# Optimization experiments

Hardware: AMD Instinct MI355X
Metric: run time of the kernel (lower is better)

## Reference

```python
import jax, jax.numpy as jnp
import numpy as np

NUM_CLASSES = 512  # P distinct identities in the batch (labels are in [0, P))
TAU = 0.5
EPS = 1e-12


def _l2norm(x):
    # F.normalize(x, dim=1) with eps clamp
    n = jnp.sqrt(jnp.sum(x * x, axis=1, keepdims=True))
    return x / jnp.maximum(n, EPS)


def setup_inputs() -> dict:
    key = jax.random.key(0)
    k1, k2, k3 = jax.random.split(key, 3)
    N, D, P = 8192, 2048, NUM_CLASSES
    feat_vp = jax.random.normal(k1, (N, D), dtype=jnp.float32)
    feat_ap = jax.random.normal(k2, (N, D), dtype=jnp.float32)
    feat_rp = jax.random.normal(k3, (N, D), dtype=jnp.float32)
    # P identities, K = N/P instances each; every class present
    label = (jnp.arange(N) % P).astype(jnp.int32)
    return {"feat_vp": feat_vp, "feat_ap": feat_ap, "feat_rp": feat_rp, "label": label}


def reference(feat_vp, feat_ap, feat_rp, label):
    P = NUM_CLASSES
    fv = _l2norm(feat_vp)
    fa = _l2norm(feat_ap)
    fr = _l2norm(feat_rp)

    # segment-mean over labels (replaces the O(N^2 D) python loop)
    counts = jax.ops.segment_sum(jnp.ones_like(label, dtype=fv.dtype), label,
                                 num_segments=P)  # [P]
    inv_cnt = 1.0 / counts[:, None]

    def centers(f):
        s = jax.ops.segment_sum(f, label, num_segments=P)  # [P, D]
        return _l2norm(s * inv_cnt)

    cv, ca, cr = centers(fv), centers(fa), centers(fr)

    # per-sample centers = unique centers gathered back by label
    loss_intra = (jnp.sum((fv - cv[label]) ** 2, axis=1).mean()
                  + jnp.sum((fa - ca[label]) ** 2, axis=1).mean()
                  + jnp.sum((fr - cr[label]) ** 2, axis=1).mean())

    def pair_loss(c1, c2):
        logits = (c1 @ c2.T) / TAU  # [P, P]
        logp = jax.nn.log_softmax(logits, axis=1)
        return -jnp.mean(jnp.diagonal(logp))

    loss_inter = pair_loss(cv, ca) + pair_loss(cv, cr) + pair_loss(ca, cr)
    return loss_intra + loss_inter
```

## Files before the change

kernel.cpp:

```cpp
#include <hip/hip_runtime.h>
#include <hip/hip_bf16.h>

#define P_CLS 512
#define D_DIM 2048
#define CAP   32
#define TAU_INV 2.0f

typedef short short8 __attribute__((ext_vector_type(8)));
typedef float f32x4 __attribute__((ext_vector_type(4)));

__device__ __forceinline__ unsigned short f2bf_bits(float x) {
  __hip_bfloat16 b = __float2bfloat16(x);
  unsigned short u;
  __builtin_memcpy(&u, &b, sizeof(u));
  return u;
}

__device__ __forceinline__ void async16(const void* g, void* l) {
  __builtin_amdgcn_global_load_lds(
      (const __attribute__((address_space(1))) void*)g,
      (__attribute__((address_space(3))) void*)l, 16, 0, 0);
}

__device__ __forceinline__ float xred_sum(float v) {
#pragma unroll
  for (int o = 1; o < 64; o <<= 1) v += __shfl_xor(v, o, 64);
  return v;
}
__device__ __forceinline__ float xred_max(float v) {
#pragma unroll
  for (int o = 1; o < 64; o <<= 1) v = fmaxf(v, __shfl_xor(v, o, 64));
  return v;
}

__global__ void k_init(int* cnt, float* accs) {
  int t = blockIdx.x * blockDim.x + threadIdx.x;
  if (t < P_CLS) cnt[t] = 0;
  if (t < 8) accs[t] = 0.f;
}

__global__ void k_index(const int* __restrict__ label, int* __restrict__ cnt,
                        int* __restrict__ idx, int n) {
  int i = blockIdx.x * blockDim.x + threadIdx.x;
  if (i < n) {
    int p = label[i];
    int slot = atomicAdd(&cnt[p], 1);
    if (slot < CAP) idx[p * CAP + slot] = i;
  }
}

__global__ __launch_bounds__(256)
void k_centers(const float* __restrict__ f0, const float* __restrict__ f1,
               const float* __restrict__ f2, const int* __restrict__ cnt,
               const int* __restrict__ idx, __hip_bfloat16* __restrict__ cb,
               float* __restrict__ accs) {
  __shared__ __align__(16) float rows[8 * D_DIM];
  __shared__ float scr[16];
  int p = blockIdx.x, m = blockIdx.y;
  const float* F = (m == 0) ? f0 : (m == 1) ? f1 : f2;
  int t = threadIdx.x, lane = t & 63, wv = t >> 6;
  int c = cnt[p];
  if (c > CAP) c = CAP;
  const int* idxp = idx + p * CAP;

  f32x4 acc0 = {0, 0, 0, 0}, acc1 = {0, 0, 0, 0};
  for (int base = 0; base < c; base += 8) {
#pragma unroll
    for (int s = 0; s < 2; ++s) {
      int rr = 2 * wv + s, gr = base + rr;
      if (gr < c) {
        const char* rowp = (const char*)(F + (long)idxp[gr] * D_DIM);
        char* ldsp = (char*)(rows + rr * D_DIM);
#pragma unroll
        for (int j = 0; j < 8; ++j)
          async16(rowp + j * 1024 + lane * 16, ldsp + j * 1024 + lane * 16);
      }
    }
    __syncthreads();
#pragma unroll
    for (int s = 0; s < 2; ++s) {
      int rr = 2 * wv + s;
      const f32x4* rp = (const f32x4*)(rows + rr * D_DIM);
      float ssq = 0.f;
#pragma unroll
      for (int j = 0; j < 8; ++j) {
        f32x4 q = rp[lane + 64 * j];
        q = q * q;
        ssq += q.x + q.y + q.z + q.w;
      }
      ssq = xred_sum(ssq);
      if (lane == 0)
        scr[rr] = (base + rr < c) ? (1.0f / fmaxf(sqrtf(ssq), 1e-12f)) : 0.f;
    }
    __syncthreads();
#pragma unroll
    for (int rr = 0; rr < 8; ++rr) {
      float w = scr[rr];
      f32x4 x0 = *(const f32x4*)(rows + rr * D_DIM + t * 4);
      f32x4 x1 = *(const f32x4*)(rows + rr * D_DIM + 1024 + t * 4);
      acc0 += x0 * w;
      acc1 += x1 * w;
    }
    __syncthreads();
  }
  f32x4 q0 = acc0 * acc0, q1 = acc1 * acc1;
  float s2 = q0.x + q0.y + q0.z + q0.w + q1.x + q1.y + q1.z + q1.w;
  s2 = xred_sum(s2);
  if (lane == 0) scr[8 + wv] = s2;
  __syncthreads();
  s2 = scr[8] + scr[9] + scr[10] + scr[11];
  float sn = sqrtf(s2);
  float inv = 1.0f / fmaxf(sn, 1e-12f);
  __hip_bfloat16* dst = cb + ((long)m * P_CLS + p) * D_DIM;
  f32x4 o0 = acc0 * inv, o1 = acc1 * inv;
  ushort4 h0, h1;
  h0.x = f2bf_bits(o0.x); h0.y = f2bf_bits(o0.y);
  h0.z = f2bf_bits(o0.z); h0.w = f2bf_bits(o0.w);
  h1.x = f2bf_bits(o1.x); h1.y = f2bf_bits(o1.y);
  h1.z = f2bf_bits(o1.z); h1.w = f2bf_bits(o1.w);
  ((ushort4*)dst)[t] = h0;
  ((ushort4*)dst)[t + 256] = h1;
  if (t == 0 && c > 0) atomicAdd(&accs[0], sn);
}

__global__ __launch_bounds__(256)
void k_gemm(const __hip_bfloat16* __restrict__ cbh, float* __restrict__ logits) {
  __shared__ __align__(16) unsigned short As[2][64 * 40], Bs[2][64 * 40];
  int pair = blockIdx.y, kz = blockIdx.z, nkz = gridDim.z;
  int ksl = D_DIM / nkz;
  int ma = (pair == 2) ? 1 : 0;
  int mb = (pair == 0) ? 1 : 2;
  const unsigned short* A =
      (const unsigned short*)cbh + (long)ma * P_CLS * D_DIM + kz * ksl;
  const unsigned short* B =
      (const unsigned short*)cbh + (long)mb * P_CLS * D_DIM + kz * ksl;
  float* C = logits + ((long)kz * 3 + pair) * P_CLS * P_CLS;
  int tm = (blockIdx.x >> 3) * 64, tn = (blockIdx.x & 7) * 64;
  int t = threadIdx.x, lane = t & 63, wv = t >> 6;
  int srow = t >> 2, skc = (t & 3) * 8;
  int quad = lane >> 4, mr = lane & 15;
  const unsigned short* pa = A + (long)(tm + srow) * D_DIM + skc;
  const unsigned short* pb = B + (long)(tn + srow) * D_DIM + skc;
  f32x4 acc[4] = {{0,0,0,0},{0,0,0,0},{0,0,0,0},{0,0,0,0}};
  uint4 av = *(const uint4*)pa, bv = *(const uint4*)pb;
  *(uint4*)(&As[0][srow * 40 + skc]) = av;
  *(uint4*)(&Bs[0][srow * 40 + skc]) = bv;
  av = *(const uint4*)(pa + 32); bv = *(const uint4*)(pb + 32);
  const int NIT = ksl / 32;
  for (int it = 0; it < NIT; ++it) {
    __syncthreads();
    int cur = it & 1;
    if (it + 1 < NIT) {
      *(uint4*)(&As[cur ^ 1][srow * 40 + skc]) = av;
      *(uint4*)(&Bs[cur ^ 1][srow * 40 + skc]) = bv;
    }
    if (it + 2 < NIT) {
      av = *(const uint4*)(pa + (it + 2) * 32);
      bv = *(const uint4*)(pb + (it + 2) * 32);
    }
    short8 af = *(const short8*)(&As[cur][(wv * 16 + mr) * 40 + quad * 8]);
#pragma unroll
    for (int nb = 0; nb < 4; ++nb) {
      short8 bfr = *(const short8*)(&Bs[cur][(nb * 16 + mr) * 40 + quad * 8]);
      acc[nb] = __builtin_amdgcn_mfma_f32_16x16x32_bf16(af, bfr, acc[nb], 0, 0, 0);
    }
  }
  int crow = tm + wv * 16 + quad * 4;
#pragma unroll
  for (int nb = 0; nb < 4; ++nb)
#pragma unroll
    for (int r = 0; r < 4; ++r)
      C[(long)(crow + r) * P_CLS + tn + nb * 16 + mr] = acc[nb][r] * TAU_INV;
}

__global__ __launch_bounds__(256)
void k_lse(const float* __restrict__ logits, float* __restrict__ accs, int nkz) {
  __shared__ float sred[8];
  int row = blockIdx.x;
  int p = row & (P_CLS - 1);
  int t = threadIdx.x, lane = t & 63, wv = t >> 6;
  float v0 = 0.f, v1 = 0.f, diag = 0.f;
  for (int z = 0; z < nkz; ++z) {
    const float* L = logits + ((long)z * 3 * P_CLS + row) * P_CLS;
    v0 += L[t];
    v1 += L[t + 256];
  }
  float mx = xred_max(fmaxf(v0, v1));
  if (lane == 0) sred[wv] = mx;
  __syncthreads();
  mx = fmaxf(fmaxf(sred[0], sred[1]), fmaxf(sred[2], sred[3]));
  float e = expf(v0 - mx) + expf(v1 - mx);
  e = xred_sum(e);
  if (lane == 0) sred[4 + wv] = e;
  __syncthreads();
  if (t == 0) {
    float tot = sred[4] + sred[5] + sred[6] + sred[7];
    for (int z = 0; z < nkz; ++z)
      diag += logits[((long)z * 3 * P_CLS + row) * P_CLS + p];
    atomicAdd(&accs[1], mx + logf(tot) - diag);
  }
}

__global__ void k_final(const float* __restrict__ accs, float* __restrict__ out,
                        float invN) {
  out[0] = 6.0f - 2.0f * invN * accs[0] + accs[1] * (1.0f / (float)P_CLS);
}

extern "C" void kernel_launch(void* const* d_in, const int* in_sizes, int n_in,
                              void* d_out, int out_size, void* d_ws, size_t ws_size,
                              hipStream_t stream) {
  const float* fvp = (const float*)d_in[0];
  const float* fap = (const float*)d_in[1];
  const float* frp = (const float*)d_in[2];
  const int* label = (const int*)d_in[3];
  int N = in_sizes[3];

  char* ws = (char*)d_ws;
  int* cnt = (int*)ws;
  int* idx = (int*)(ws + 2048);
  float* accs = (float*)(ws + 2048 + 65536);
  __hip_bfloat16* cb = (__hip_bfloat16*)(ws + 131072);
  float* logits = (float*)(ws + 131072 + 3ul * P_CLS * D_DIM * 2);

  size_t base = 131072 + 3ul * P_CLS * D_DIM * 2;
  size_t per_z = 3ul * P_CLS * P_CLS * 4;
  int KZ = (ws_size >= base + 4 * per_z) ? 4 : 2;

  hipLaunchKernelGGL(k_init, dim3(1), dim3(512), 0, stream, cnt, accs);
  hipLaunchKernelGGL(k_index, dim3((N + 255) / 256), dim3(256), 0, stream,
                     label, cnt, idx, N);
  hipLaunchKernelGGL(k_centers, dim3(P_CLS, 3), dim3(256), 0, stream,
                     fvp, fap, frp, cnt, idx, cb, accs);
  hipLaunchKernelGGL(k_gemm, dim3(64, 3, KZ), dim3(256), 0, stream, cb, logits);
  hipLaunchKernelGGL(k_lse, dim3(3 * P_CLS), dim3(256), 0, stream, logits, accs, KZ);
  hipLaunchKernelGGL(k_final, dim3(1), dim3(1), 0, stream, accs, (float*)d_out,
                     1.0f / (float)N);
}
```

Before: 239.7 us.

## Fuse init/index kernels, stream center rows via registers, fold final into LSE

Merges the init and index kernels into one single-block kernel that counts with LDS atomics, and folds the final-combine kernel into the LSE kernel using a last-block-done counter, so two launches are removed. The centers kernel stops staging rows in LDS with async loads. Each thread now streams its columns of every member row straight into registers, prefetching two rows ahead, and needs one block barrier per row to get the norm. This cuts LDS use and raises occupancy, but adds a barrier per row and makes the label indexing serial on one block.

```diff
diff --git a/kernel.cpp b/kernel.cpp
--- a/kernel.cpp
+++ b/kernel.cpp
@@ -16,12 +16,6 @@
   return u;
 }
 
-__device__ __forceinline__ void async16(const void* g, void* l) {
-  __builtin_amdgcn_global_load_lds(
-      (const __attribute__((address_space(1))) void*)g,
-      (__attribute__((address_space(3))) void*)l, 16, 0, 0);
-}
-
 __device__ __forceinline__ float xred_sum(float v) {
 #pragma unroll
   for (int o = 1; o < 64; o <<= 1) v += __shfl_xor(v, o, 64);
@@ -33,20 +27,21 @@
   return v;
 }
 
-__global__ void k_init(int* cnt, float* accs) {
-  int t = blockIdx.x * blockDim.x + threadIdx.x;
-  if (t < P_CLS) cnt[t] = 0;
-  if (t < 8) accs[t] = 0.f;
-}
-
-__global__ void k_index(const int* __restrict__ label, int* __restrict__ cnt,
-                        int* __restrict__ idx, int n) {
-  int i = blockIdx.x * blockDim.x + threadIdx.x;
-  if (i < n) {
+__global__ __launch_bounds__(1024)
+void k_prep(const int* __restrict__ label, int* __restrict__ cnt,
+            int* __restrict__ idx, float* __restrict__ accs, int n) {
+  __shared__ int lcnt[P_CLS];
+  int t = threadIdx.x;
+  if (t < P_CLS) lcnt[t] = 0;
+  if (t >= P_CLS && t < P_CLS + 8) accs[t - P_CLS] = 0.f;
+  __syncthreads();
+  for (int i = t; i < n; i += 1024) {
     int p = label[i];
-    int slot = atomicAdd(&cnt[p], 1);
+    int slot = atomicAdd(&lcnt[p], 1);
     if (slot < CAP) idx[p * CAP + slot] = i;
   }
+  __syncthreads();
+  if (t < P_CLS) cnt[t] = lcnt[t];
 }
 
 __global__ __launch_bounds__(256)
@@ -54,62 +49,52 @@
                const float* __restrict__ f2, const int* __restrict__ cnt,
                const int* __restrict__ idx, __hip_bfloat16* __restrict__ cb,
                float* __restrict__ accs) {
-  __shared__ __align__(16) float rows[8 * D_DIM];
-  __shared__ float scr[16];
+  __shared__ float scr[2][4];
+  __shared__ float s2s[4];
   int p = blockIdx.x, m = blockIdx.y;
   const float* F = (m == 0) ? f0 : (m == 1) ? f1 : f2;
   int t = threadIdx.x, lane = t & 63, wv = t >> 6;
   int c = cnt[p];
   if (c > CAP) c = CAP;
   const int* idxp = idx + p * CAP;
-
+  int col0 = wv * 512 + lane * 4;
   f32x4 acc0 = {0, 0, 0, 0}, acc1 = {0, 0, 0, 0};
-  for (int base = 0; base < c; base += 8) {
-#pragma unroll
-    for (int s = 0; s < 2; ++s) {
-      int rr = 2 * wv + s, gr = base + rr;
-      if (gr < c) {
-        const char* rowp = (const char*)(F + (long)idxp[gr] * D_DIM);
-        char* ldsp = (char*)(rows + rr * D_DIM);
-#pragma unroll
-        for (int j = 0; j < 8; ++j)
-          async16(rowp + j * 1024 + lane * 16, ldsp + j * 1024 + lane * 16);
+  if (c > 0) {
+    const float* rp0 = F + (long)idxp[0] * D_DIM;
+    f32x4 v0 = *(const f32x4*)(rp0 + col0);
+    f32x4 v1 = *(const f32x4*)(rp0 + col0 + 256);
+    f32x4 n10 = {0,0,0,0}, n11 = {0,0,0,0};
+    if (c > 1) {
+      const float* rp1 = F + (long)idxp[1] * D_DIM;
+      n10 = *(const f32x4*)(rp1 + col0);
+      n11 = *(const f32x4*)(rp1 + col0 + 256);
+    }
+    for (int r = 0; r < c; ++r) {
+      f32x4 n20 = {0,0,0,0}, n21 = {0,0,0,0};
+      if (r + 2 < c) {
+        const float* rp2 = F + (long)idxp[r + 2] * D_DIM;
+        n20 = *(const f32x4*)(rp2 + col0);
+        n21 = *(const f32x4*)(rp2 + col0 + 256);
       }
-    }
-    __syncthreads();
-#pragma unroll
-    for (int s = 0; s < 2; ++s) {
-      int rr = 2 * wv + s;
-      const f32x4* rp = (const f32x4*)(rows + rr * D_DIM);
-      float ssq = 0.f;
-#pragma unroll
-      for (int j = 0; j < 8; ++j) {
-        f32x4 q = rp[lane + 64 * j];
-        q = q * q;
-        ssq += q.x + q.y + q.z + q.w;
-      }
+      f32x4 q = v0 * v0 + v1 * v1;
+      float ssq = q.x + q.y + q.z + q.w;
       ssq = xred_sum(ssq);
-      if (lane == 0)
-        scr[rr] = (base + rr < c) ? (1.0f / fmaxf(sqrtf(ssq), 1e-12f)) : 0.f;
-    }
-    __syncthreads();
-#pragma unroll
-    for (int rr = 0; rr < 8; ++rr) {
-      float w = scr[rr];
-      f32x4 x0 = *(const f32x4*)(rows + rr * D_DIM + t * 4);
-      f32x4 x1 = *(const f32x4*)(rows + rr * D_DIM + 1024 + t * 4);
-      acc0 += x0 * w;
-      acc1 += x1 * w;
-    }
-    __syncthreads();
-  }
-  f32x4 q0 = acc0 * acc0, q1 = acc1 * acc1;
-  float s2 = q0.x + q0.y + q0.z + q0.w + q1.x + q1.y + q1.z + q1.w;
+      if (lane == 0) scr[r & 1][wv] = ssq;
+      __syncthreads();
+      float tot = scr[r & 1][0] + scr[r & 1][1] + scr[r & 1][2] + scr[r & 1][3];
+      float w = 1.0f / fmaxf(sqrtf(tot), 1e-12f);
+      acc0 += v0 * w;
+      acc1 += v1 * w;
+      v0 = n10; v1 = n11;
+      n10 = n20; n11 = n21;
+    }
+  }
+  f32x4 q = acc0 * acc0 + acc1 * acc1;
+  float s2 = q.x + q.y + q.z + q.w;
   s2 = xred_sum(s2);
-  if (lane == 0) scr[8 + wv] = s2;
-  __syncthreads();
-  s2 = scr[8] + scr[9] + scr[10] + scr[11];
-  float sn = sqrtf(s2);
+  if (lane == 0) s2s[wv] = s2;
+  __syncthreads();
+  float sn = sqrtf(s2s[0] + s2s[1] + s2s[2] + s2s[3]);
   float inv = 1.0f / fmaxf(sn, 1e-12f);
   __hip_bfloat16* dst = cb + ((long)m * P_CLS + p) * D_DIM;
   f32x4 o0 = acc0 * inv, o1 = acc1 * inv;
@@ -118,8 +103,8 @@
   h0.z = f2bf_bits(o0.z); h0.w = f2bf_bits(o0.w);
   h1.x = f2bf_bits(o1.x); h1.y = f2bf_bits(o1.y);
   h1.z = f2bf_bits(o1.z); h1.w = f2bf_bits(o1.w);
-  ((ushort4*)dst)[t] = h0;
-  ((ushort4*)dst)[t + 256] = h1;
+  *(ushort4*)(dst + col0) = h0;
+  *(ushort4*)(dst + col0 + 256) = h1;
   if (t == 0 && c > 0) atomicAdd(&accs[0], sn);
 }
 
@@ -174,12 +159,13 @@
 }
 
 __global__ __launch_bounds__(256)
-void k_lse(const float* __restrict__ logits, float* __restrict__ accs, int nkz) {
+void k_lse(const float* __restrict__ logits, float* __restrict__ accs, int nkz,
+           float* __restrict__ out, float invN) {
   __shared__ float sred[8];
   int row = blockIdx.x;
   int p = row & (P_CLS - 1);
   int t = threadIdx.x, lane = t & 63, wv = t >> 6;
-  float v0 = 0.f, v1 = 0.f, diag = 0.f;
+  float v0 = 0.f, v1 = 0.f;
   for (int z = 0; z < nkz; ++z) {
     const float* L = logits + ((long)z * 3 * P_CLS + row) * P_CLS;
     v0 += L[t];
@@ -195,15 +181,18 @@
   __syncthreads();
   if (t == 0) {
     float tot = sred[4] + sred[5] + sred[6] + sred[7];
+    float diag = 0.f;
     for (int z = 0; z < nkz; ++z)
       diag += logits[((long)z * 3 * P_CLS + row) * P_CLS + p];
     atomicAdd(&accs[1], mx + logf(tot) - diag);
-  }
-}
-
-__global__ void k_final(const float* __restrict__ accs, float* __restrict__ out,
-                        float invN) {
-  out[0] = 6.0f - 2.0f * invN * accs[0] + accs[1] * (1.0f / (float)P_CLS);
+    __threadfence();
+    int old = atomicAdd((int*)&accs[2], 1);
+    if (old == gridDim.x - 1) {
+      float li = atomicAdd(&accs[1], 0.f);
+      float ls = atomicAdd(&accs[0], 0.f);
+      out[0] = 6.0f - 2.0f * invN * ls + li * (1.0f / (float)P_CLS);
+    }
+  }
 }
 
 extern "C" void kernel_launch(void* const* d_in, const int* in_sizes, int n_in,
@@ -226,13 +215,11 @@
   size_t per_z = 3ul * P_CLS * P_CLS * 4;
   int KZ = (ws_size >= base + 4 * per_z) ? 4 : 2;
 
-  hipLaunchKernelGGL(k_init, dim3(1), dim3(512), 0, stream, cnt, accs);
-  hipLaunchKernelGGL(k_index, dim3((N + 255) / 256), dim3(256), 0, stream,
-                     label, cnt, idx, N);
+  hipLaunchKernelGGL(k_prep, dim3(1), dim3(1024), 0, stream, label, cnt, idx,
+                     accs, N);
   hipLaunchKernelGGL(k_centers, dim3(P_CLS, 3), dim3(256), 0, stream,
                      fvp, fap, frp, cnt, idx, cb, accs);
   hipLaunchKernelGGL(k_gemm, dim3(64, 3, KZ), dim3(256), 0, stream, cb, logits);
-  hipLaunchKernelGGL(k_lse, dim3(3 * P_CLS), dim3(256), 0, stream, logits, accs, KZ);
-  hipLaunchKernelGGL(k_final, dim3(1), dim3(1), 0, stream, accs, (float*)d_out,
-                     1.0f / (float)N);
-}
+  hipLaunchKernelGGL(k_lse, dim3(3 * P_CLS), dim3(256), 0, stream, logits, accs,
+                     KZ, (float*)d_out, 1.0f / (float)N);
+}
```

Measured after the change: 269.3 us. 1.12x slower.
